# Kernel tuning notes

Hardware: AMD Instinct MI355X
Metric: run time of the kernel (lower is better)

Reference implementation:

```python
import jax, jax.numpy as jnp
import numpy as np

NUM_EXPERTS = 2
TOP_K = 2


def setup_inputs() -> dict:
    key = jax.random.key(0)
    ks = jax.random.split(key, 5)
    B, T, M, H, E = 8, 512, 2048, 1024, NUM_EXPERTS
    x = jax.random.normal(ks[0], (B, T, M), dtype=jnp.float32)
    wg = jax.random.normal(ks[1], (M, E), dtype=jnp.float32) * 0.02
    w1 = jax.random.normal(ks[2], (E, M, H), dtype=jnp.float32) * 0.02
    b1 = jnp.zeros((E, H), dtype=jnp.float32)
    w2 = jax.random.normal(ks[3], (E, H, M), dtype=jnp.float32) * 0.02
    b2 = jnp.zeros((E, M), dtype=jnp.float32)
    return {"x": x, "wg": wg, "w1": w1, "b1": b1, "w2": w2, "b2": b2}


def _moe_forward(x, wg, w1, b1, w2, b2):
    B, T, M = x.shape
    E = wg.shape[1]
    S = B * T
    C = TOP_K * ((S + E - 1) // E)  # GShard top-2 capacity, factor 1.0
    xf = x.reshape(S, M)

    # --- fp32 gate (Top2Gate) ---
    logits = jnp.einsum('sm,me->se', xf.astype(jnp.float32), wg.astype(jnp.float32))
    gates = jax.nn.softmax(logits, axis=-1)  # [S,E]

    idx1 = jnp.argmax(gates, axis=-1)
    mask1 = jax.nn.one_hot(idx1, E, dtype=jnp.float32)
    gates_wo1 = jnp.where(mask1 > 0, -jnp.inf, logits)
    idx2 = jnp.argmax(gates_wo1, axis=-1)
    mask2 = jax.nn.one_hot(idx2, E, dtype=jnp.float32)

    # positions within each expert's buffer
    loc1 = jnp.cumsum(mask1, axis=0) - 1.0                      # [S,E]
    loc2 = jnp.cumsum(mask2, axis=0) - 1.0 + jnp.sum(mask1, axis=0, keepdims=True)
    mask1 = mask1 * (loc1 < C)
    mask2 = mask2 * (loc2 < C)

    g1 = jnp.sum(gates * mask1, axis=1)  # [S]
    g2 = jnp.sum(gates * mask2, axis=1)
    denom = jnp.maximum(g1 + g2, jnp.finfo(jnp.float32).eps)
    g1, g2 = g1 / denom, g2 / denom

    p1 = jnp.sum(loc1 * mask1, axis=1).astype(jnp.int32)  # capacity slot per token
    p2 = jnp.sum(loc2 * mask2, axis=1).astype(jnp.int32)
    oh1 = jax.nn.one_hot(p1, C, dtype=jnp.float32)  # [S,C]
    oh2 = jax.nn.one_hot(p2, C, dtype=jnp.float32)

    combine = (g1[:, None, None] * mask1[:, :, None] * oh1[:, None, :]
               + g2[:, None, None] * mask2[:, :, None] * oh2[:, None, :])  # [S,E,C]
    dispatch = (combine > 0).astype(xf.dtype)

    # --- dispatch, grouped expert FFN, combine ---
    disp = jnp.einsum('sec,sm->ecm', dispatch, xf)                 # [E,C,M]
    h = jax.nn.relu(jnp.einsum('ecm,emh->ech', disp, w1) + b1[:, None, :])
    y = jnp.einsum('ech,ehm->ecm', h, w2) + b2[:, None, :]         # [E,C,M]
    out = jnp.einsum('sec,ecm->sm', combine.astype(xf.dtype), y)   # [S,M]
    return out.reshape(B, T, M)


def reference(x, wg, w1, b1, w2, b2):
    moe_out = _moe_forward(x, wg, w1, b1, w2, b2)          # [B,T,M]
    summed = jnp.sum(moe_out, axis=2)                      # [B,T]
    return jax.nn.log_softmax(summed, axis=1)
```

## Files before the change

### kernel.cpp

```cpp
#include <hip/hip_runtime.h>

typedef unsigned short u16;
typedef unsigned int   u32;
typedef u16   u16x4 __attribute__((ext_vector_type(4)));
typedef u16   u16x8 __attribute__((ext_vector_type(8)));
typedef short s16x8 __attribute__((ext_vector_type(8)));
typedef float f32x4 __attribute__((ext_vector_type(4)));

#define S_TOK 4096
#define MDIM  2048
#define NDIM  2048
#define HDIM  1024
#define TDIM  512

__device__ __forceinline__ u16 f2bf(float f) {
  u32 u = __float_as_uint(f);
  u = u + 0x7fffu + ((u >> 16) & 1u);
  return (u16)(u >> 16);
}

__device__ __forceinline__ void gl2lds16(const void* g, void* l) {
  __builtin_amdgcn_global_load_lds(
      (const __attribute__((address_space(1))) void*)g,
      (__attribute__((address_space(3))) void*)l, 16, 0, 0);
}

__global__ __launch_bounds__(256) void prep_w1t(const float* __restrict__ w1,
                                                u16* __restrict__ w1t) {
  __shared__ float tile[32][33];
  int bid = blockIdx.x;
  int e   = bid >> 11;
  int idx = bid & 2047;
  int m0  = (idx >> 5) << 5;
  int h0  = (idx & 31) << 5;
  int t = threadIdx.x;
  int r = t >> 3, q = t & 7;
  const float* src = w1 + ((size_t)e * MDIM + (m0 + r)) * HDIM + h0 + q * 4;
  f32x4 v = *(const f32x4*)src;
  tile[r][q*4+0] = v[0]; tile[r][q*4+1] = v[1];
  tile[r][q*4+2] = v[2]; tile[r][q*4+3] = v[3];
  __syncthreads();
  u16x4 o;
  o[0] = f2bf(tile[q*4+0][r]);
  o[1] = f2bf(tile[q*4+1][r]);
  o[2] = f2bf(tile[q*4+2][r]);
  o[3] = f2bf(tile[q*4+3][r]);
  u16* dst = w1t + ((size_t)e * HDIM + (h0 + r)) * MDIM + m0 + q * 4;
  *(u16x4*)dst = o;
}

__global__ __launch_bounds__(256) void prep_sums(const float* __restrict__ w2,
                                                 const float* __restrict__ b2,
                                                 float* __restrict__ w2sum,
                                                 float* __restrict__ b2sum) {
  int row  = blockIdx.x * 4 + (threadIdx.x >> 6);
  int lane = threadIdx.x & 63;
  const float* src;
  if (row < NDIM)          src = w2 + (size_t)row * MDIM;
  else if (row < NDIM + 2) src = b2 + (size_t)(row - NDIM) * MDIM;
  else return;
  float acc = 0.f;
  for (int m = lane * 4; m < MDIM; m += 256) {
    f32x4 v = *(const f32x4*)(src + m);
    acc += v[0] + v[1] + v[2] + v[3];
  }
  #pragma unroll
  for (int off = 32; off; off >>= 1) acc += __shfl_xor(acc, off);
  if (lane == 0) {
    if (row < NDIM) w2sum[row] = acc;
    else            b2sum[row - NDIM] = acc;
  }
}

__global__ __launch_bounds__(256) void gate_xbf(const float* __restrict__ x,
                                                const float* __restrict__ wg,
                                                float* __restrict__ g,
                                                u16* __restrict__ xbf) {
  int s    = blockIdx.x * 4 + (threadIdx.x >> 6);
  int lane = threadIdx.x & 63;
  const float* xr = x + (size_t)s * MDIM;
  u16* xbr = xbf + (size_t)s * MDIM;
  float l0 = 0.f, l1 = 0.f;
  for (int m = lane * 4; m < MDIM; m += 256) {
    f32x4 xv = *(const f32x4*)(xr + m);
    f32x4 wa = *(const f32x4*)(wg + 2 * m);
    f32x4 wb = *(const f32x4*)(wg + 2 * m + 4);
    l0 += xv[0]*wa[0] + xv[1]*wa[2] + xv[2]*wb[0] + xv[3]*wb[2];
    l1 += xv[0]*wa[1] + xv[1]*wa[3] + xv[2]*wb[1] + xv[3]*wb[3];
    u16x4 o; o[0]=f2bf(xv[0]); o[1]=f2bf(xv[1]); o[2]=f2bf(xv[2]); o[3]=f2bf(xv[3]);
    *(u16x4*)(xbr + m) = o;
  }
  #pragma unroll
  for (int off = 32; off; off >>= 1) {
    l0 += __shfl_xor(l0, off);
    l1 += __shfl_xor(l1, off);
  }
  if (lane == 0) {
    float mx = fmaxf(l0, l1);
    float e0 = expf(l0 - mx), e1 = expf(l1 - mx);
    float inv = 1.f / (e0 + e1);
    g[2*s]   = e0 * inv;
    g[2*s+1] = e1 * inv;
  }
}

#define BM 128
#define BN 128
#define BK 64
#define KT (MDIM / BK)

__global__ __launch_bounds__(512, 4) void gemm_fused(const u16* __restrict__ xbf,
                                                     const u16* __restrict__ w1t,
                                                     const float* __restrict__ b1,
                                                     const float* __restrict__ w2sum,
                                                     float* __restrict__ ssum) {
  __shared__ u16 As[2][BM * BK];
  __shared__ u16 Bs[2][BN * BK];

  int bid  = blockIdx.x;
  int tile = (bid & 7) * 64 + (bid >> 3);
  int bn = tile & 15;
  int bm = tile >> 4;
  int gs0 = bm * BM;
  int gn0 = bn * BN;

  int tid  = threadIdx.x;
  int lane = tid & 63;
  int wid  = tid >> 6;
  int wr = wid >> 2, wc = wid & 3;
  int fr = lane & 15, fg = lane >> 4;

  int lr = lane >> 3;
  int lc = (lane & 7) ^ lr;
  int row0 = wid * 16;
  const u16* asrc = xbf + (size_t)(gs0 + row0 + lr) * MDIM + lc * 8;
  const u16* bsrc = w1t + (size_t)(gn0 + row0 + lr) * MDIM + lc * 8;

  f32x4 acc[4][2] = {};

  {
    gl2lds16(asrc,            &As[0][ row0      * BK]);
    gl2lds16(asrc + 8 * MDIM, &As[0][(row0 + 8) * BK]);
    gl2lds16(bsrc,            &Bs[0][ row0      * BK]);
    gl2lds16(bsrc + 8 * MDIM, &Bs[0][(row0 + 8) * BK]);
  }

  for (int kt = 0; kt < KT; ++kt) {
    int cur = kt & 1;
    __syncthreads();
    if (kt + 1 < KT) {
      int k0 = (kt + 1) * BK;
      gl2lds16(asrc + k0,            &As[cur ^ 1][ row0      * BK]);
      gl2lds16(asrc + k0 + 8 * MDIM, &As[cur ^ 1][(row0 + 8) * BK]);
      gl2lds16(bsrc + k0,            &Bs[cur ^ 1][ row0      * BK]);
      gl2lds16(bsrc + k0 + 8 * MDIM, &Bs[cur ^ 1][(row0 + 8) * BK]);
    }
    #pragma unroll
    for (int kk = 0; kk < 2; ++kk) {
      s16x8 af[4], bfr[2];
      #pragma unroll
      for (int i = 0; i < 4; ++i) {
        int row = wr * 64 + i * 16 + fr;
        int ch  = (fg + 4 * kk) ^ (fr & 7);
        af[i] = *(const s16x8*)(&As[cur][row * BK + ch * 8]);
      }
      #pragma unroll
      for (int j = 0; j < 2; ++j) {
        int row = wc * 32 + j * 16 + fr;
        int ch  = (fg + 4 * kk) ^ (fr & 7);
        bfr[j] = *(const s16x8*)(&Bs[cur][row * BK + ch * 8]);
      }
      #pragma unroll
      for (int i = 0; i < 4; ++i)
        #pragma unroll
        for (int j = 0; j < 2; ++j)
          acc[i][j] = __builtin_amdgcn_mfma_f32_16x16x32_bf16(af[i], bfr[j], acc[i][j], 0, 0, 0);
    }
  }

  int e = gn0 >> 10;
  float b1v[2], w2v[2];
  #pragma unroll
  for (int j = 0; j < 2; ++j) {
    int n = gn0 + wc * 32 + j * 16 + fr;
    b1v[j] = b1[n];
    w2v[j] = w2sum[n];
  }
  #pragma unroll
  for (int i = 0; i < 4; ++i) {
    #pragma unroll
    for (int r = 0; r < 4; ++r) {
      float sv = 0.f;
      #pragma unroll
      for (int j = 0; j < 2; ++j)
        sv += fmaxf(acc[i][j][r] + b1v[j], 0.f) * w2v[j];
      sv += __shfl_xor(sv, 1);
      sv += __shfl_xor(sv, 2);
      sv += __shfl_xor(sv, 4);
      sv += __shfl_xor(sv, 8);
      if (fr == 0) {
        int s = gs0 + wr * 64 + i * 16 + fg * 4 + r;
        atomicAdd(&ssum[(size_t)e * S_TOK + s], sv);
      }
    }
  }
}

__global__ __launch_bounds__(512) void finalize(const float* __restrict__ g,
                                                const float* __restrict__ ssum,
                                                const float* __restrict__ b2sum,
                                                float* __restrict__ out) {
  __shared__ float sA[8];
  __shared__ float sB[2];
  int b = blockIdx.x;
  int t = threadIdx.x;
  int s = b * TDIM + t;
  int lane = t & 63, wid = t >> 6;
  float g0 = g[2*s], g1 = g[2*s+1];
  float v = g0 * (ssum[s] + b2sum[0]) + g1 * (ssum[S_TOK + s] + b2sum[1]);
  float m = v;
  #pragma unroll
  for (int off = 32; off; off >>= 1) m = fmaxf(m, __shfl_xor(m, off));
  if (lane == 0) sA[wid] = m;
  __syncthreads();
  if (t == 0) {
    float mm = sA[0];
    #pragma unroll
    for (int i = 1; i < 8; ++i) mm = fmaxf(mm, sA[i]);
    sB[0] = mm;
  }
  __syncthreads();
  float gm = sB[0];
  float ex = expf(v - gm);
  float sum = ex;
  #pragma unroll
  for (int off = 32; off; off >>= 1) sum += __shfl_xor(sum, off);
  if (lane == 0) sA[wid] = sum;
  __syncthreads();
  if (t == 0) {
    float ss = 0.f;
    #pragma unroll
    for (int i = 0; i < 8; ++i) ss += sA[i];
    sB[1] = logf(ss);
  }
  __syncthreads();
  out[s] = v - gm - sB[1];
}

extern "C" void kernel_launch(void* const* d_in, const int* in_sizes, int n_in,
                              void* d_out, int out_size, void* d_ws, size_t ws_size,
                              hipStream_t stream) {
  const float* x  = (const float*)d_in[0];
  const float* wg = (const float*)d_in[1];
  const float* w1 = (const float*)d_in[2];
  const float* b1 = (const float*)d_in[3];
  const float* w2 = (const float*)d_in[4];
  const float* b2 = (const float*)d_in[5];
  float* out = (float*)d_out;

  char* ws = (char*)d_ws;
  u16*   w1t   = (u16*)ws;
  u16*   xbf   = (u16*)(ws + 8388608);
  float* ssum  = (float*)(ws + 25165824);
  float* gbuf  = (float*)(ws + 25198592);
  float* w2sum = (float*)(ws + 25231360);
  float* b2sum = (float*)(ws + 25239552);

  hipMemsetAsync(ssum, 0, S_TOK * 2 * sizeof(float), stream);
  hipLaunchKernelGGL(prep_w1t,   dim3(4096), dim3(256), 0, stream, w1, w1t);
  hipLaunchKernelGGL(prep_sums,  dim3(513),  dim3(256), 0, stream, w2, b2, w2sum, b2sum);
  hipLaunchKernelGGL(gate_xbf,   dim3(1024), dim3(256), 0, stream, x, wg, gbuf, xbf);
  hipLaunchKernelGGL(gemm_fused, dim3(512),  dim3(512), 0, stream, xbf, w1t, b1, w2sum, ssum);
  hipLaunchKernelGGL(finalize,   dim3(8),    dim3(512), 0, stream, gbuf, ssum, b2sum, out);
}
```

Before: 69.53 us.

## Merge prep kernels and restructure GEMM to 256-row tiles with phased prefetch

Merges the three preprocessing kernels into one launch with a block-range dispatch, removing two kernel launches and their serialization. The fused GEMM tile grows from 128 to 256 rows, which halves the grid and the number of times weight tiles are re-read. The K loop is split into four sub-phases, each interleaving LDS reads, staggered global-to-LDS prefetches, manual waitcnt/barriers and raised wave priority around MFMAs. The risks are higher register pressure (occupancy hint drops to 2) and fewer blocks (256) to fill the CUs.

```diff
diff --git a/kernel.cpp b/kernel.cpp
--- a/kernel.cpp
+++ b/kernel.cpp
@@ -25,91 +25,95 @@
       (__attribute__((address_space(3))) void*)l, 16, 0, 0);
 }
 
-__global__ __launch_bounds__(256) void prep_w1t(const float* __restrict__ w1,
-                                                u16* __restrict__ w1t) {
-  __shared__ float tile[32][33];
-  int bid = blockIdx.x;
-  int e   = bid >> 11;
-  int idx = bid & 2047;
-  int m0  = (idx >> 5) << 5;
-  int h0  = (idx & 31) << 5;
-  int t = threadIdx.x;
-  int r = t >> 3, q = t & 7;
-  const float* src = w1 + ((size_t)e * MDIM + (m0 + r)) * HDIM + h0 + q * 4;
-  f32x4 v = *(const f32x4*)src;
-  tile[r][q*4+0] = v[0]; tile[r][q*4+1] = v[1];
-  tile[r][q*4+2] = v[2]; tile[r][q*4+3] = v[3];
-  __syncthreads();
-  u16x4 o;
-  o[0] = f2bf(tile[q*4+0][r]);
-  o[1] = f2bf(tile[q*4+1][r]);
-  o[2] = f2bf(tile[q*4+2][r]);
-  o[3] = f2bf(tile[q*4+3][r]);
-  u16* dst = w1t + ((size_t)e * HDIM + (h0 + r)) * MDIM + m0 + q * 4;
-  *(u16x4*)dst = o;
-}
-
-__global__ __launch_bounds__(256) void prep_sums(const float* __restrict__ w2,
-                                                 const float* __restrict__ b2,
-                                                 float* __restrict__ w2sum,
-                                                 float* __restrict__ b2sum) {
-  int row  = blockIdx.x * 4 + (threadIdx.x >> 6);
-  int lane = threadIdx.x & 63;
-  const float* src;
-  if (row < NDIM)          src = w2 + (size_t)row * MDIM;
-  else if (row < NDIM + 2) src = b2 + (size_t)(row - NDIM) * MDIM;
-  else return;
-  float acc = 0.f;
-  for (int m = lane * 4; m < MDIM; m += 256) {
-    f32x4 v = *(const f32x4*)(src + m);
-    acc += v[0] + v[1] + v[2] + v[3];
-  }
-  #pragma unroll
-  for (int off = 32; off; off >>= 1) acc += __shfl_xor(acc, off);
-  if (lane == 0) {
-    if (row < NDIM) w2sum[row] = acc;
-    else            b2sum[row - NDIM] = acc;
-  }
-}
-
-__global__ __launch_bounds__(256) void gate_xbf(const float* __restrict__ x,
+__global__ __launch_bounds__(256) void prep_all(const float* __restrict__ w1,
+                                                u16* __restrict__ w1t,
+                                                const float* __restrict__ w2,
+                                                const float* __restrict__ b2,
+                                                float* __restrict__ w2sum,
+                                                float* __restrict__ b2sum,
+                                                const float* __restrict__ x,
                                                 const float* __restrict__ wg,
                                                 float* __restrict__ g,
                                                 u16* __restrict__ xbf) {
-  int s    = blockIdx.x * 4 + (threadIdx.x >> 6);
-  int lane = threadIdx.x & 63;
-  const float* xr = x + (size_t)s * MDIM;
-  u16* xbr = xbf + (size_t)s * MDIM;
-  float l0 = 0.f, l1 = 0.f;
-  for (int m = lane * 4; m < MDIM; m += 256) {
-    f32x4 xv = *(const f32x4*)(xr + m);
-    f32x4 wa = *(const f32x4*)(wg + 2 * m);
-    f32x4 wb = *(const f32x4*)(wg + 2 * m + 4);
-    l0 += xv[0]*wa[0] + xv[1]*wa[2] + xv[2]*wb[0] + xv[3]*wb[2];
-    l1 += xv[0]*wa[1] + xv[1]*wa[3] + xv[2]*wb[1] + xv[3]*wb[3];
-    u16x4 o; o[0]=f2bf(xv[0]); o[1]=f2bf(xv[1]); o[2]=f2bf(xv[2]); o[3]=f2bf(xv[3]);
-    *(u16x4*)(xbr + m) = o;
-  }
-  #pragma unroll
-  for (int off = 32; off; off >>= 1) {
-    l0 += __shfl_xor(l0, off);
-    l1 += __shfl_xor(l1, off);
-  }
-  if (lane == 0) {
-    float mx = fmaxf(l0, l1);
-    float e0 = expf(l0 - mx), e1 = expf(l1 - mx);
-    float inv = 1.f / (e0 + e1);
-    g[2*s]   = e0 * inv;
-    g[2*s+1] = e1 * inv;
-  }
-}
-
-#define BM 128
+  __shared__ float tile[32][33];
+  int b = blockIdx.x;
+  int t = threadIdx.x;
+  if (b < 4096) {
+    int e   = b >> 11;
+    int idx = b & 2047;
+    int m0  = (idx >> 5) << 5;
+    int h0  = (idx & 31) << 5;
+    int r = t >> 3, q = t & 7;
+    const float* src = w1 + ((size_t)e * MDIM + (m0 + r)) * HDIM + h0 + q * 4;
+    f32x4 v = *(const f32x4*)src;
+    tile[r][q*4+0] = v[0]; tile[r][q*4+1] = v[1];
+    tile[r][q*4+2] = v[2]; tile[r][q*4+3] = v[3];
+    __syncthreads();
+    u16x4 o;
+    o[0] = f2bf(tile[q*4+0][r]);
+    o[1] = f2bf(tile[q*4+1][r]);
+    o[2] = f2bf(tile[q*4+2][r]);
+    o[3] = f2bf(tile[q*4+3][r]);
+    u16* dst = w1t + ((size_t)e * HDIM + (h0 + r)) * MDIM + m0 + q * 4;
+    *(u16x4*)dst = o;
+  } else if (b < 4609) {
+    int bid  = b - 4096;
+    int row  = bid * 4 + (t >> 6);
+    int lane = t & 63;
+    const float* src;
+    if (row < NDIM)          src = w2 + (size_t)row * MDIM;
+    else if (row < NDIM + 2) src = b2 + (size_t)(row - NDIM) * MDIM;
+    else return;
+    float acc = 0.f;
+    for (int m = lane * 4; m < MDIM; m += 256) {
+      f32x4 v = *(const f32x4*)(src + m);
+      acc += v[0] + v[1] + v[2] + v[3];
+    }
+    #pragma unroll
+    for (int off = 32; off; off >>= 1) acc += __shfl_xor(acc, off);
+    if (lane == 0) {
+      if (row < NDIM) w2sum[row] = acc;
+      else            b2sum[row - NDIM] = acc;
+    }
+  } else {
+    int bid  = b - 4609;
+    int s    = bid * 4 + (t >> 6);
+    int lane = t & 63;
+    const float* xr = x + (size_t)s * MDIM;
+    u16* xbr = xbf + (size_t)s * MDIM;
+    float l0 = 0.f, l1 = 0.f;
+    for (int m = lane * 4; m < MDIM; m += 256) {
+      f32x4 xv = *(const f32x4*)(xr + m);
+      f32x4 wa = *(const f32x4*)(wg + 2 * m);
+      f32x4 wb = *(const f32x4*)(wg + 2 * m + 4);
+      l0 += xv[0]*wa[0] + xv[1]*wa[2] + xv[2]*wb[0] + xv[3]*wb[2];
+      l1 += xv[0]*wa[1] + xv[1]*wa[3] + xv[2]*wb[1] + xv[3]*wb[3];
+      u16x4 o; o[0]=f2bf(xv[0]); o[1]=f2bf(xv[1]); o[2]=f2bf(xv[2]); o[3]=f2bf(xv[3]);
+      *(u16x4*)(xbr + m) = o;
+    }
+    #pragma unroll
+    for (int off = 32; off; off >>= 1) {
+      l0 += __shfl_xor(l0, off);
+      l1 += __shfl_xor(l1, off);
+    }
+    if (lane == 0) {
+      float mx = fmaxf(l0, l1);
+      float e0 = expf(l0 - mx), e1 = expf(l1 - mx);
+      float inv = 1.f / (e0 + e1);
+      g[2*s]   = e0 * inv;
+      g[2*s+1] = e1 * inv;
+    }
+  }
+}
+
+#define BM 256
 #define BN 128
 #define BK 64
 #define KT (MDIM / BK)
 
-__global__ __launch_bounds__(512, 4) void gemm_fused(const u16* __restrict__ xbf,
+#define MFMA_BF16 __builtin_amdgcn_mfma_f32_16x16x32_bf16
+
+__global__ __launch_bounds__(512, 2) void gemm_fused(const u16* __restrict__ xbf,
                                                      const u16* __restrict__ w1t,
                                                      const float* __restrict__ b1,
                                                      const float* __restrict__ w2sum,
@@ -118,9 +122,9 @@
   __shared__ u16 Bs[2][BN * BK];
 
   int bid  = blockIdx.x;
-  int tile = (bid & 7) * 64 + (bid >> 3);
+  int tile = (bid & 7) * 32 + (bid >> 3);
+  int bm = tile >> 4;
   int bn = tile & 15;
-  int bm = tile >> 4;
   int gs0 = bm * BM;
   int gn0 = bn * BN;
 
@@ -132,49 +136,115 @@
 
   int lr = lane >> 3;
   int lc = (lane & 7) ^ lr;
-  int row0 = wid * 16;
-  const u16* asrc = xbf + (size_t)(gs0 + row0 + lr) * MDIM + lc * 8;
-  const u16* bsrc = w1t + (size_t)(gn0 + row0 + lr) * MDIM + lc * 8;
-
-  f32x4 acc[4][2] = {};
+  const u16* aS = xbf + (size_t)(gs0 + wid * 8 + lr) * MDIM + lc * 8;
+  const u16* bS = w1t + (size_t)(gn0 + wid * 8 + lr) * MDIM + lc * 8;
+  int aD = wid * 8 * BK;
+  int bD = wid * 8 * BK;
+
+  int ch0 = (fg ^ (fr & 7)) * 8;
+  int aOff[8], bOff[2];
+  #pragma unroll
+  for (int i = 0; i < 8; ++i) {
+    int rb = (i < 4) ? (wr * 64 + i * 16) : (128 + wr * 64 + (i - 4) * 16);
+    aOff[i] = (rb + fr) * BK + ch0;
+  }
+  #pragma unroll
+  for (int j = 0; j < 2; ++j) bOff[j] = (wc * 32 + j * 16 + fr) * BK + ch0;
+
+  f32x4 acc[8][2] = {};
 
   {
-    gl2lds16(asrc,            &As[0][ row0      * BK]);
-    gl2lds16(asrc + 8 * MDIM, &As[0][(row0 + 8) * BK]);
-    gl2lds16(bsrc,            &Bs[0][ row0      * BK]);
-    gl2lds16(bsrc + 8 * MDIM, &Bs[0][(row0 + 8) * BK]);
-  }
-
-  for (int kt = 0; kt < KT; ++kt) {
-    int cur = kt & 1;
-    __syncthreads();
-    if (kt + 1 < KT) {
-      int k0 = (kt + 1) * BK;
-      gl2lds16(asrc + k0,            &As[cur ^ 1][ row0      * BK]);
-      gl2lds16(asrc + k0 + 8 * MDIM, &As[cur ^ 1][(row0 + 8) * BK]);
-      gl2lds16(bsrc + k0,            &Bs[cur ^ 1][ row0      * BK]);
-      gl2lds16(bsrc + k0 + 8 * MDIM, &Bs[cur ^ 1][(row0 + 8) * BK]);
-    }
-    #pragma unroll
-    for (int kk = 0; kk < 2; ++kk) {
-      s16x8 af[4], bfr[2];
+    u16* An = &As[0][0];
+    u16* Bn = &Bs[0][0];
+    gl2lds16(bS,              Bn + bD);
+    gl2lds16(bS + 64 * MDIM,  Bn + bD + 64 * BK);
+    gl2lds16(aS,              An + aD);
+    gl2lds16(aS + 64 * MDIM,  An + aD + 64 * BK);
+    gl2lds16(aS + 128 * MDIM, An + aD + 128 * BK);
+    gl2lds16(aS + 192 * MDIM, An + aD + 192 * BK);
+  }
+
+  for (int t = 0; t < KT; ++t) {
+    const u16* Ac = &As[t & 1][0];
+    const u16* Bc = &Bs[t & 1][0];
+    u16* An = &As[(t & 1) ^ 1][0];
+    u16* Bn = &Bs[(t & 1) ^ 1][0];
+    int nk = (t + 1) * BK;
+    bool notlast = (t + 1 < KT);
+
+    s16x8 b0, b1f;
+
+    if (notlast) asm volatile("s_waitcnt vmcnt(2)" ::: "memory");
+    else         asm volatile("s_waitcnt vmcnt(0)" ::: "memory");
+    asm volatile("s_barrier" ::: "memory");
+    {
+      s16x8 a[4];
+      #pragma unroll
+      for (int i = 0; i < 4; ++i) a[i] = *(const s16x8*)(Ac + aOff[i]);
+      b0  = *(const s16x8*)(Bc + bOff[0]);
+      b1f = *(const s16x8*)(Bc + bOff[1]);
+      if (notlast) {
+        gl2lds16(bS + nk,             Bn + bD);
+        gl2lds16(bS + nk + 64 * MDIM, Bn + bD + 64 * BK);
+      }
+      __builtin_amdgcn_s_setprio(1);
       #pragma unroll
       for (int i = 0; i < 4; ++i) {
-        int row = wr * 64 + i * 16 + fr;
-        int ch  = (fg + 4 * kk) ^ (fr & 7);
-        af[i] = *(const s16x8*)(&As[cur][row * BK + ch * 8]);
-      }
-      #pragma unroll
-      for (int j = 0; j < 2; ++j) {
-        int row = wc * 32 + j * 16 + fr;
-        int ch  = (fg + 4 * kk) ^ (fr & 7);
-        bfr[j] = *(const s16x8*)(&Bs[cur][row * BK + ch * 8]);
-      }
-      #pragma unroll
-      for (int i = 0; i < 4; ++i)
-        #pragma unroll
-        for (int j = 0; j < 2; ++j)
-          acc[i][j] = __builtin_amdgcn_mfma_f32_16x16x32_bf16(af[i], bfr[j], acc[i][j], 0, 0, 0);
+        acc[i][0] = MFMA_BF16(a[i], b0,  acc[i][0], 0, 0, 0);
+        acc[i][1] = MFMA_BF16(a[i], b1f, acc[i][1], 0, 0, 0);
+      }
+      __builtin_amdgcn_s_setprio(0);
+    }
+    if (notlast) asm volatile("s_waitcnt vmcnt(2)" ::: "memory");
+    else         asm volatile("s_waitcnt vmcnt(0)" ::: "memory");
+    asm volatile("s_barrier" ::: "memory");
+    {
+      s16x8 a[4];
+      #pragma unroll
+      for (int i = 0; i < 4; ++i) a[i] = *(const s16x8*)(Ac + aOff[4 + i]);
+      if (notlast) {
+        gl2lds16(aS + nk,             An + aD);
+        gl2lds16(aS + nk + 64 * MDIM, An + aD + 64 * BK);
+      }
+      __builtin_amdgcn_s_setprio(1);
+      #pragma unroll
+      for (int i = 0; i < 4; ++i) {
+        acc[4 + i][0] = MFMA_BF16(a[i], b0,  acc[4 + i][0], 0, 0, 0);
+        acc[4 + i][1] = MFMA_BF16(a[i], b1f, acc[4 + i][1], 0, 0, 0);
+      }
+      __builtin_amdgcn_s_setprio(0);
+    }
+    asm volatile("s_barrier" ::: "memory");
+    {
+      s16x8 a[4];
+      #pragma unroll
+      for (int i = 0; i < 4; ++i) a[i] = *(const s16x8*)(Ac + (aOff[i] ^ 32));
+      b0  = *(const s16x8*)(Bc + (bOff[0] ^ 32));
+      b1f = *(const s16x8*)(Bc + (bOff[1] ^ 32));
+      if (notlast) {
+        gl2lds16(aS + nk + 128 * MDIM, An + aD + 128 * BK);
+        gl2lds16(aS + nk + 192 * MDIM, An + aD + 192 * BK);
+      }
+      __builtin_amdgcn_s_setprio(1);
+      #pragma unroll
+      for (int i = 0; i < 4; ++i) {
+        acc[i][0] = MFMA_BF16(a[i], b0,  acc[i][0], 0, 0, 0);
+        acc[i][1] = MFMA_BF16(a[i], b1f, acc[i][1], 0, 0, 0);
+      }
+      __builtin_amdgcn_s_setprio(0);
+    }
+    asm volatile("s_barrier" ::: "memory");
+    {
+      s16x8 a[4];
+      #pragma unroll
+      for (int i = 0; i < 4; ++i) a[i] = *(const s16x8*)(Ac + (aOff[4 + i] ^ 32));
+      __builtin_amdgcn_s_setprio(1);
+      #pragma unroll
+      for (int i = 0; i < 4; ++i) {
+        acc[4 + i][0] = MFMA_BF16(a[i], b0,  acc[4 + i][0], 0, 0, 0);
+        acc[4 + i][1] = MFMA_BF16(a[i], b1f, acc[4 + i][1], 0, 0, 0);
+      }
+      __builtin_amdgcn_s_setprio(0);
     }
   }
 
@@ -187,19 +257,18 @@
     w2v[j] = w2sum[n];
   }
   #pragma unroll
-  for (int i = 0; i < 4; ++i) {
+  for (int i = 0; i < 8; ++i) {
+    int rb = (i < 4) ? (wr * 64 + i * 16) : (128 + wr * 64 + (i - 4) * 16);
     #pragma unroll
     for (int r = 0; r < 4; ++r) {
-      float sv = 0.f;
-      #pragma unroll
-      for (int j = 0; j < 2; ++j)
-        sv += fmaxf(acc[i][j][r] + b1v[j], 0.f) * w2v[j];
+      float sv = fmaxf(acc[i][0][r] + b1v[0], 0.f) * w2v[0]
+               + fmaxf(acc[i][1][r] + b1v[1], 0.f) * w2v[1];
       sv += __shfl_xor(sv, 1);
       sv += __shfl_xor(sv, 2);
       sv += __shfl_xor(sv, 4);
       sv += __shfl_xor(sv, 8);
       if (fr == 0) {
-        int s = gs0 + wr * 64 + i * 16 + fg * 4 + r;
+        int s = gs0 + rb + fg * 4 + r;
         atomicAdd(&ssum[(size_t)e * S_TOK + s], sv);
       }
     }
@@ -267,9 +336,8 @@
   float* b2sum = (float*)(ws + 25239552);
 
   hipMemsetAsync(ssum, 0, S_TOK * 2 * sizeof(float), stream);
-  hipLaunchKernelGGL(prep_w1t,   dim3(4096), dim3(256), 0, stream, w1, w1t);
-  hipLaunchKernelGGL(prep_sums,  dim3(513),  dim3(256), 0, stream, w2, b2, w2sum, b2sum);
-  hipLaunchKernelGGL(gate_xbf,   dim3(1024), dim3(256), 0, stream, x, wg, gbuf, xbf);
-  hipLaunchKernelGGL(gemm_fused, dim3(512),  dim3(512), 0, stream, xbf, w1t, b1, w2sum, ssum);
+  hipLaunchKernelGGL(prep_all,   dim3(5633), dim3(256), 0, stream,
+                     w1, w1t, w2, b2, w2sum, b2sum, x, wg, gbuf, xbf);
+  hipLaunchKernelGGL(gemm_fused, dim3(256),  dim3(512), 0, stream, xbf, w1t, b1, w2sum, ssum);
   hipLaunchKernelGGL(finalize,   dim3(8),    dim3(512), 0, stream, gbuf, ssum, b2sum, out);
 }
```

New measurement: 75.04 us. 1.08x slower.
